# Kernel optimization log

Hardware: AMD Instinct MI355X
Metric: run time of the kernel (lower is better)

Reference implementation:

```python
import jax, jax.numpy as jnp
import numpy as np

N_NODES = 100000


def setup_inputs() -> dict:
    key = jax.random.key(0)
    k1, k2, k3, k4 = jax.random.split(key, 4)
    h = jax.random.normal(k1, (N_NODES, 128), dtype=jnp.float32)
    src = jax.random.randint(k2, (1600000,), 0, N_NODES, dtype=jnp.int32)
    dst = jax.random.randint(k3, (1600000,), 0, N_NODES, dtype=jnp.int32)
    # Linear params (PyTorch default init scale ~ 1/sqrt(in_feats))
    W = jax.random.normal(k4, (128, 128), dtype=jnp.float32) * (1.0 / np.sqrt(128.0))
    b = jnp.zeros((128,), dtype=jnp.float32)
    return {"h": h, "src": src, "dst": dst, "W": W, "b": b}


def reference(h, src, dst, W, b):
    # fn.copy_src: gather source-node features per edge  [E, F]
    msgs = h[src]
    # fn.sum: scatter-add messages into destination nodes  [N, F]
    agg = jax.ops.segment_sum(msgs, dst, num_segments=h.shape[0])
    # NodeUpdateModule: linear + relu
    out = agg @ W.T + b
    return jax.nn.relu(out)
```

## Files before the change

kernel.cpp:

```cpp
#include <hip/hip_runtime.h>

#define F      128
#define NPB    256
#define NPBS   8
#define NBMAX  512
#define ECAP   5120
#define CHMAX  4096
#define CH_PT  4
#define OVFCAP 32768
#define BR     64
#define KC     32

typedef short bf16x8 __attribute__((ext_vector_type(8)));
typedef float f32x4  __attribute__((ext_vector_type(4)));

__device__ __forceinline__ unsigned short f32_to_bf16_rne(float x) {
    unsigned u = __float_as_uint(x);
    u += 0x7fffu + ((u >> 16) & 1u);
    return (unsigned short)(u >> 16);
}

__global__ __launch_bounds__(256) void conv_w_kernel(
        const float* __restrict__ Wf, unsigned short* __restrict__ Wb, int n4) {
    int i = blockIdx.x * blockDim.x + threadIdx.x;
    if (i < n4) {
        float4 v = *(const float4*)(Wf + 4 * (long)i);
        ushort4 o;
        o.x = f32_to_bf16_rne(v.x);
        o.y = f32_to_bf16_rne(v.y);
        o.z = f32_to_bf16_rne(v.z);
        o.w = f32_to_bf16_rne(v.w);
        *(ushort4*)(Wb + 4 * (long)i) = o;
    }
}

__global__ __launch_bounds__(256) void gemm_h_kernel(
        const float* __restrict__ h,
        const unsigned short* __restrict__ Wb,
        unsigned short* __restrict__ hp,
        int n_rows) {
    __shared__ unsigned short a_lds[64][136];
    const int tid = threadIdx.x;
    const int r0 = blockIdx.x * 64;
    if (r0 >= n_rows) return;

    #pragma unroll
    for (int k = 0; k < 8; ++k) {
        int idx = k * 256 + tid;
        int row = idx >> 5;
        int c4 = idx & 31;
        int grow = min(r0 + row, n_rows - 1);
        float4 v = *(const float4*)(h + (long)grow * F + c4 * 4);
        ushort4 o;
        o.x = f32_to_bf16_rne(v.x);
        o.y = f32_to_bf16_rne(v.y);
        o.z = f32_to_bf16_rne(v.z);
        o.w = f32_to_bf16_rne(v.w);
        *(ushort4*)&a_lds[row][c4 * 4] = o;
    }
    __syncthreads();

    const int wv = tid >> 6;
    const int lane = tid & 63;
    const int mn = lane & 15;
    const int quad = lane >> 4;
    const int m0 = r0 + wv * 16;
    if (m0 >= n_rows) return;

    bf16x8 afr[4];
    #pragma unroll
    for (int kk = 0; kk < 4; ++kk)
        afr[kk] = *(const bf16x8*)&a_lds[wv * 16 + mn][kk * 32 + quad * 8];

    f32x4 acc[8];
    #pragma unroll
    for (int t = 0; t < 8; ++t) acc[t] = (f32x4){0.f, 0.f, 0.f, 0.f};

    #pragma unroll
    for (int kk = 0; kk < 4; ++kk) {
        #pragma unroll
        for (int t = 0; t < 8; ++t) {
            const unsigned short* wp = Wb + (long)(t * 16 + mn) * F + kk * 32 + quad * 8;
            bf16x8 bfr = *(const bf16x8*)wp;
            acc[t] = __builtin_amdgcn_mfma_f32_16x16x32_bf16(afr[kk], bfr, acc[t], 0, 0, 0);
        }
    }

    #pragma unroll
    for (int t = 0; t < 8; ++t) {
        const int col = t * 16 + mn;
        #pragma unroll
        for (int r = 0; r < 4; ++r) {
            const int orow = m0 + quad * 4 + r;
            if (orow < n_rows)
                hp[(long)orow * F + col] = f32_to_bf16_rne(acc[t][r]);
        }
    }
}

__global__ __launch_bounds__(1024) void count_kernel(
        const int* __restrict__ dst,
        int* __restrict__ cntmat,
        int n_edges, int NB) {
    __shared__ int hist[NBMAX];
    const int tid = threadIdx.x;
    const int lo = blockIdx.x * CHMAX;
    const int hi = min(n_edges, lo + CHMAX);
    for (int i = tid; i < NB; i += 1024) hist[i] = 0;
    __syncthreads();
    for (int i = lo + tid; i < hi; i += 1024)
        atomicAdd(&hist[((unsigned)dst[i]) >> NPBS], 1);
    __syncthreads();
    int* row = cntmat + (long)blockIdx.x * NB;
    for (int i = tid; i < NB; i += 1024) row[i] = hist[i];
}

__global__ __launch_bounds__(256) void scan_kernel(
        int* __restrict__ cntmat, int* __restrict__ gcnt, int NB, int NBLK) {
    __shared__ int wsum[4];
    const int b = blockIdx.x;
    const int tid = threadIdx.x;
    const int lane = tid & 63;
    const int w = tid >> 6;
    int carry = 0;
    for (int c0 = 0; c0 < NBLK; c0 += 256) {
        const int blk = c0 + tid;
        const int own = (blk < NBLK) ? cntmat[(long)blk * NB + b] : 0;
        int v = own;
        #pragma unroll
        for (int d = 1; d < 64; d <<= 1) { int u = __shfl_up(v, d); if (lane >= d) v += u; }
        if (lane == 63) wsum[w] = v;
        __syncthreads();
        if (w == 0) {
            int s = (lane < 4) ? wsum[lane] : 0;
            #pragma unroll
            for (int d = 1; d < 4; d <<= 1) { int u = __shfl_up(s, d); if (lane >= d) s += u; }
            if (lane < 4) wsum[lane] = s;
        }
        __syncthreads();
        const int excl = v - own + ((w > 0) ? wsum[w - 1] : 0) + carry;
        if (blk < NBLK) cntmat[(long)blk * NB + b] = excl;
        carry += wsum[3];
        __syncthreads();
    }
    if (tid == 0) gcnt[b] = carry;
}

__global__ __launch_bounds__(1024) void scatter_kernel(
        const int* __restrict__ src,
        const int* __restrict__ dst,
        const int* __restrict__ cntmat,
        int* __restrict__ ebuf,
        int* __restrict__ ovf,
        int n_edges, int NB) {
    __shared__ int hist[NBMAX];
    __shared__ int dlt[NBMAX];
    __shared__ int cursor[NBMAX];
    __shared__ int sval[CHMAX];
    __shared__ unsigned short sbkt[CHMAX];
    __shared__ int wsum[16];
    const int tid = threadIdx.x;
    const int lane = tid & 63;
    const int w = tid >> 6;
    const int lo = blockIdx.x * CHMAX;
    const int hi = min(n_edges, lo + CHMAX);
    const int len = hi - lo;

    int dd[CH_PT], ss[CH_PT];
    #pragma unroll
    for (int k = 0; k < CH_PT; ++k) {
        int i = lo + k * 1024 + tid;
        bool ok = i < hi;
        dd[k] = ok ? dst[i] : -1;
        ss[k] = ok ? src[i] : 0;
    }
    for (int i = tid; i < NB; i += 1024) hist[i] = 0;
    __syncthreads();

    #pragma unroll
    for (int k = 0; k < CH_PT; ++k)
        if (dd[k] >= 0) atomicAdd(&hist[((unsigned)dd[k]) >> NPBS], 1);
    __syncthreads();

    const int own = (tid < NB) ? hist[tid] : 0;
    int v = own;
    #pragma unroll
    for (int d = 1; d < 64; d <<= 1) { int u = __shfl_up(v, d); if (lane >= d) v += u; }
    if (lane == 63) wsum[w] = v;
    __syncthreads();
    if (w == 0) {
        int s = (lane < 16) ? wsum[lane] : 0;
        #pragma unroll
        for (int d = 1; d < 16; d <<= 1) { int u = __shfl_up(s, d); if (lane >= d) s += u; }
        if (lane < 16) wsum[lane] = s;
    }
    __syncthreads();
    if (tid < NB) {
        const int excl = v - own + ((w > 0) ? wsum[w - 1] : 0);
        dlt[tid] = cntmat[(long)blockIdx.x * NB + tid] - excl;
        cursor[tid] = excl;
    }
    __syncthreads();

    #pragma unroll
    for (int k = 0; k < CH_PT; ++k)
        if (dd[k] >= 0) {
            int b = ((unsigned)dd[k]) >> NPBS;
            int p = atomicAdd(&cursor[b], 1);
            sval[p] = ((dd[k] & (NPB - 1)) << 20) | ss[k];
            sbkt[p] = (unsigned short)b;
        }
    __syncthreads();

    for (int i = tid; i < len; i += 1024) {
        int vv = sval[i];
        int b = sbkt[i];
        int slot = i + dlt[b];
        if (slot < ECAP) {
            ebuf[(long)b * ECAP + slot] = vv;
        } else {
            int q = atomicAdd(&ovf[0], 1);
            if (q < OVFCAP) {
                ovf[1 + 2 * q] = (b << NPBS) | (vv >> 20);
                ovf[2 + 2 * q] = vv & 0xFFFFF;
            }
        }
    }
}

__global__ __launch_bounds__(1024) void bucket_gather_kernel(
        const unsigned short* __restrict__ hp,
        const int* __restrict__ gcnt,
        const int* __restrict__ ebuf,
        const int* __restrict__ ovf,
        const float* __restrict__ bias,
        float* __restrict__ out,
        int n_nodes) {
    __shared__ int hist[NPB];
    __shared__ int ofs[NPB];
    __shared__ int cur[NPB];
    __shared__ int srt[ECAP];
    __shared__ int wsum[16];
    const int bkt = blockIdx.x;
    const int tid = threadIdx.x;
    const int lane = tid & 63;
    const int w = tid >> 6;
    const int cnt = min(gcnt[bkt], ECAP);
    const int novf = ovf[0];
    const int* eb = ebuf + (long)bkt * ECAP;

    int ev[5];
    #pragma unroll
    for (int k = 0; k < 5; ++k) {
        int i = k * 1024 + tid;
        ev[k] = (i < cnt) ? eb[i] : -1;
    }
    if (tid < NPB) hist[tid] = 0;
    __syncthreads();

    #pragma unroll
    for (int k = 0; k < 5; ++k)
        if (ev[k] >= 0) atomicAdd(&hist[((unsigned)ev[k]) >> 20], 1);
    __syncthreads();

    const int own = (tid < NPB) ? hist[tid] : 0;
    int v = own;
    #pragma unroll
    for (int d = 1; d < 64; d <<= 1) { int u = __shfl_up(v, d); if (lane >= d) v += u; }
    if (lane == 63) wsum[w] = v;
    __syncthreads();
    if (w == 0) {
        int s = (lane < 16) ? wsum[lane] : 0;
        #pragma unroll
        for (int d = 1; d < 16; d <<= 1) { int u = __shfl_up(s, d); if (lane >= d) s += u; }
        if (lane < 16) wsum[lane] = s;
    }
    __syncthreads();
    if (tid < NPB) {
        const int e = v - own + ((w > 0) ? wsum[w - 1] : 0);
        ofs[tid] = e;
        cur[tid] = e;
    }
    __syncthreads();

    #pragma unroll
    for (int k = 0; k < 5; ++k)
        if (ev[k] >= 0) {
            int p = atomicAdd(&cur[((unsigned)ev[k]) >> 20], 1);
            srt[p] = ev[k] & 0xFFFFF;
        }
    __syncthreads();

    const unsigned lo4 = lane << 2;
    const float2 bv = *(const float2*)(bias + (lane << 1));
    for (int nl = w; nl < NPB; nl += 32) {
        const int nA = (bkt << NPBS) + nl;
        const int nB = nA + 16;
        if (nA >= n_nodes) break;
        const int begA = ofs[nl];
        const int lenA = hist[nl];
        const int begB = ofs[nl + 16];
        const int lenB = hist[nl + 16];
        const int fbA = (lenA > 0) ? begA : begB;
        const int fbB = (lenB > 0) ? begB : begA;
        const int mx = max(lenA, lenB);

        float ax0 = 0.f, ay0 = 0.f, ax1 = 0.f, ay1 = 0.f;
        for (int i = 0; i < mx; i += 8) {
            unsigned va[8], vb[8];
            bool la[8], lb[8];
            #pragma unroll
            for (int j = 0; j < 8; ++j) {
                la[j] = (i + j) < lenA;
                lb[j] = (i + j) < lenB;
                int sa = srt[la[j] ? begA + i + j : fbA];
                int sb = srt[lb[j] ? begB + i + j : fbB];
                va[j] = *(const unsigned*)((const char*)hp +
                                           (((unsigned)sa << 8) | lo4));
                vb[j] = *(const unsigned*)((const char*)hp +
                                           (((unsigned)sb << 8) | lo4));
            }
            #pragma unroll
            for (int j = 0; j < 8; ++j) {
                if (la[j]) {
                    ax0 += __uint_as_float(va[j] << 16);
                    ay0 += __uint_as_float(va[j] & 0xffff0000u);
                }
                if (lb[j]) {
                    ax1 += __uint_as_float(vb[j] << 16);
                    ay1 += __uint_as_float(vb[j] & 0xffff0000u);
                }
            }
        }

        if (novf > 0) {
            int ne = min(novf, OVFCAP);
            for (int k = 0; k < ne; ++k) {
                int dd = ovf[1 + 2 * k];
                if (dd == nA || dd == nB) {
                    unsigned u = *(const unsigned*)((const char*)hp +
                                   (((unsigned)ovf[2 + 2 * k] << 8) | lo4));
                    float ux = __uint_as_float(u << 16);
                    float uy = __uint_as_float(u & 0xffff0000u);
                    if (dd == nA) { ax0 += ux; ay0 += uy; }
                    else          { ax1 += ux; ay1 += uy; }
                }
            }
        }

        float rx0 = fmaxf(ax0 + bv.x, 0.f);
        float ry0 = fmaxf(ay0 + bv.y, 0.f);
        *(float2*)((char*)out + (((unsigned)nA << 9) | (lane << 3))) =
            make_float2(rx0, ry0);
        if (nB < n_nodes) {
            float rx1 = fmaxf(ax1 + bv.x, 0.f);
            float ry1 = fmaxf(ay1 + bv.y, 0.f);
            *(float2*)((char*)out + (((unsigned)nB << 9) | (lane << 3))) =
                make_float2(rx1, ry1);
        }
    }
}

__global__ void scatter_add_kernel(const float* __restrict__ h,
                                   const int* __restrict__ src,
                                   const int* __restrict__ dst,
                                   float* __restrict__ agg,
                                   long total) {
    long stride = (long)gridDim.x * blockDim.x;
    for (long i = (long)blockIdx.x * blockDim.x + threadIdx.x; i < total; i += stride) {
        int e    = (int)(i >> 5);
        int lane = (int)(i & 31);
        int s = src[e];
        int d = dst[e];
        float4 v = *(const float4*)(h + (long)s * F + (lane << 2));
        float* o = agg + (long)d * F + (lane << 2);
        unsafeAtomicAdd(o + 0, v.x);
        unsafeAtomicAdd(o + 1, v.y);
        unsafeAtomicAdd(o + 2, v.z);
        unsafeAtomicAdd(o + 3, v.w);
    }
}

__global__ __launch_bounds__(256) void gemm_bias_relu_inplace(
        float* __restrict__ out,
        const float* __restrict__ W,
        const float* __restrict__ bias,
        int n_rows) {
    __shared__ __align__(16) float a_t[KC][BR + 4];
    __shared__ __align__(16) float w_t[KC][F + 4];
    const int tid = threadIdx.x;
    const int tx = tid & 15;
    const int ty = tid >> 4;
    const int row0 = blockIdx.x * BR;
    float acc[4][8];
    #pragma unroll
    for (int i = 0; i < 4; ++i)
        #pragma unroll
        for (int j = 0; j < 8; ++j) acc[i][j] = 0.f;
    for (int kc = 0; kc < F; kc += KC) {
        #pragma unroll
        for (int p = 0; p < 2; ++p) {
            int q = tid + p * 256, r = q >> 3, kq = q & 7;
            int row = row0 + r;
            float4 v = make_float4(0.f, 0.f, 0.f, 0.f);
            if (row < n_rows) v = *(const float4*)(out + (long)row * F + kc + (kq << 2));
            a_t[kq * 4 + 0][r] = v.x; a_t[kq * 4 + 1][r] = v.y;
            a_t[kq * 4 + 2][r] = v.z; a_t[kq * 4 + 3][r] = v.w;
        }
        #pragma unroll
        for (int p = 0; p < 4; ++p) {
            int q = tid + p * 256, j = q >> 3, kq = q & 7;
            float4 v = *(const float4*)(W + (long)j * F + kc + (kq << 2));
            w_t[kq * 4 + 0][j] = v.x; w_t[kq * 4 + 1][j] = v.y;
            w_t[kq * 4 + 2][j] = v.z; w_t[kq * 4 + 3][j] = v.w;
        }
        __syncthreads();
        #pragma unroll
        for (int k = 0; k < KC; ++k) {
            float4 av = *(const float4*)&a_t[k][ty << 2];
            float4 w0 = *(const float4*)&w_t[k][tx << 2];
            float4 w1 = *(const float4*)&w_t[k][64 + (tx << 2)];
            float a4[4] = {av.x, av.y, av.z, av.w};
            float wv[8] = {w0.x, w0.y, w0.z, w0.w, w1.x, w1.y, w1.z, w1.w};
            #pragma unroll
            for (int i = 0; i < 4; ++i)
                #pragma unroll
                for (int j = 0; j < 8; ++j) acc[i][j] += a4[i] * wv[j];
        }
        __syncthreads();
    }
    float4 b0 = *(const float4*)(bias + (tx << 2));
    float4 b1 = *(const float4*)(bias + 64 + (tx << 2));
    #pragma unroll
    for (int i = 0; i < 4; ++i) {
        int row = row0 + (ty << 2) + i;
        if (row < n_rows) {
            float4 r0, r1;
            r0.x = fmaxf(acc[i][0] + b0.x, 0.f); r0.y = fmaxf(acc[i][1] + b0.y, 0.f);
            r0.z = fmaxf(acc[i][2] + b0.z, 0.f); r0.w = fmaxf(acc[i][3] + b0.w, 0.f);
            r1.x = fmaxf(acc[i][4] + b1.x, 0.f); r1.y = fmaxf(acc[i][5] + b1.y, 0.f);
            r1.z = fmaxf(acc[i][6] + b1.z, 0.f); r1.w = fmaxf(acc[i][7] + b1.w, 0.f);
            *(float4*)(out + (long)row * F + (tx << 2)) = r0;
            *(float4*)(out + (long)row * F + 64 + (tx << 2)) = r1;
        }
    }
}

extern "C" void kernel_launch(void* const* d_in, const int* in_sizes, int n_in,
                              void* d_out, int out_size, void* d_ws, size_t ws_size,
                              hipStream_t stream) {
    const float* h   = (const float*)d_in[0];
    const int*   src = (const int*)d_in[1];
    const int*   dst = (const int*)d_in[2];
    const float* W   = (const float*)d_in[3];
    const float* b   = (const float*)d_in[4];
    float* out = (float*)d_out;

    const int n_nodes = in_sizes[0] / F;
    const int n_edges = in_sizes[1];
    const int NB   = (n_nodes + NPB - 1) >> NPBS;
    const int NBLK = (n_edges + CHMAX - 1) / CHMAX;

    auto al16 = [](size_t x) { return (x + 15) & ~(size_t)15; };
    const size_t off_gcnt = 0;
    const size_t off_ovf  = al16((size_t)NB * 4);
    const size_t off_cmat = al16(off_ovf + 4 + (size_t)OVFCAP * 8);
    const size_t off_ebuf = al16(off_cmat + (size_t)NBLK * NB * 4);
    const size_t off_hp   = al16(off_ebuf + (size_t)NB * ECAP * 4);
    const size_t off_wb   = al16(off_hp + (size_t)n_nodes * F * 2);
    const size_t need     = off_wb + (size_t)F * F * 2;

    if (ws_size >= need && n_nodes > 0 && NB <= NBMAX) {
        int* gcnt = (int*)((char*)d_ws + off_gcnt);
        int* ovf  = (int*)((char*)d_ws + off_ovf);
        int* cmat = (int*)((char*)d_ws + off_cmat);
        int* ebuf = (int*)((char*)d_ws + off_ebuf);
        unsigned short* hp = (unsigned short*)((char*)d_ws + off_hp);
        unsigned short* Wb = (unsigned short*)((char*)d_ws + off_wb);

        hipMemsetAsync(ovf, 0, 4, stream);

        conv_w_kernel<<<(F * F / 4 + 255) / 256, 256, 0, stream>>>(W, Wb, F * F / 4);

        gemm_h_kernel<<<(n_nodes + 63) / 64, 256, 0, stream>>>(h, Wb, hp, n_nodes);

        if (NBLK > 0)
            count_kernel<<<NBLK, 1024, 0, stream>>>(dst, cmat, n_edges, NB);

        scan_kernel<<<NB, 256, 0, stream>>>(cmat, gcnt, NB, NBLK);

        if (NBLK > 0)
            scatter_kernel<<<NBLK, 1024, 0, stream>>>(src, dst, cmat, ebuf, ovf,
                                                      n_edges, NB);

        bucket_gather_kernel<<<NB, 1024, 0, stream>>>(hp, gcnt, ebuf, ovf, b,
                                                      out, n_nodes);
    } else {
        hipMemsetAsync(out, 0, (size_t)out_size * sizeof(float), stream);
        scatter_add_kernel<<<16384, 256, 0, stream>>>(
            h, src, dst, out, (long)n_edges * 32);
        const int gblocks = (n_nodes + BR - 1) / BR;
        gemm_bias_relu_inplace<<<gblocks, 256, 0, stream>>>(out, W, b, n_nodes);
    }
}
```

Baseline: 224.3 us.

## Fuse weight conversion and memset into count kernel; widen gather to 16-byte loads

```diff
diff --git a/kernel.cpp b/kernel.cpp
--- a/kernel.cpp
+++ b/kernel.cpp
@@ -20,18 +20,43 @@
     return (unsigned short)(u >> 16);
 }
 
-__global__ __launch_bounds__(256) void conv_w_kernel(
-        const float* __restrict__ Wf, unsigned short* __restrict__ Wb, int n4) {
-    int i = blockIdx.x * blockDim.x + threadIdx.x;
-    if (i < n4) {
-        float4 v = *(const float4*)(Wf + 4 * (long)i);
-        ushort4 o;
-        o.x = f32_to_bf16_rne(v.x);
-        o.y = f32_to_bf16_rne(v.y);
-        o.z = f32_to_bf16_rne(v.z);
-        o.w = f32_to_bf16_rne(v.w);
-        *(ushort4*)(Wb + 4 * (long)i) = o;
-    }
+__global__ __launch_bounds__(1024) void count_kernel(
+        const float* __restrict__ Wf,
+        unsigned short* __restrict__ Wb,
+        unsigned short* __restrict__ hp,
+        int* __restrict__ ovf,
+        const int* __restrict__ dst,
+        int* __restrict__ cntmat,
+        int n_edges, int NB, int n_nodes) {
+    const int tid = threadIdx.x;
+
+    if (blockIdx.x == 0) {
+        #pragma unroll
+        for (int k = 0; k < 4; ++k) {
+            int i = k * 1024 + tid;
+            float4 v = *(const float4*)(Wf + 4 * (long)i);
+            ushort4 o;
+            o.x = f32_to_bf16_rne(v.x);
+            o.y = f32_to_bf16_rne(v.y);
+            o.z = f32_to_bf16_rne(v.z);
+            o.w = f32_to_bf16_rne(v.w);
+            *(ushort4*)(Wb + 4 * (long)i) = o;
+        }
+        if (tid < 64) ((int*)(hp + (size_t)n_nodes * F))[tid] = 0;
+        if (tid == 0) ovf[0] = 0;
+        return;
+    }
+
+    __shared__ int hist[NBMAX];
+    const int lo = (blockIdx.x - 1) * CHMAX;
+    const int hi = min(n_edges, lo + CHMAX);
+    for (int i = tid; i < NB; i += 1024) hist[i] = 0;
+    __syncthreads();
+    for (int i = lo + tid; i < hi; i += 1024)
+        atomicAdd(&hist[((unsigned)dst[i]) >> NPBS], 1);
+    __syncthreads();
+    int* row = cntmat + (long)(blockIdx.x - 1) * NB;
+    for (int i = tid; i < NB; i += 1024) row[i] = hist[i];
 }
 
 __global__ __launch_bounds__(256) void gemm_h_kernel(
@@ -96,23 +121,6 @@
                 hp[(long)orow * F + col] = f32_to_bf16_rne(acc[t][r]);
         }
     }
-}
-
-__global__ __launch_bounds__(1024) void count_kernel(
-        const int* __restrict__ dst,
-        int* __restrict__ cntmat,
-        int n_edges, int NB) {
-    __shared__ int hist[NBMAX];
-    const int tid = threadIdx.x;
-    const int lo = blockIdx.x * CHMAX;
-    const int hi = min(n_edges, lo + CHMAX);
-    for (int i = tid; i < NB; i += 1024) hist[i] = 0;
-    __syncthreads();
-    for (int i = lo + tid; i < hi; i += 1024)
-        atomicAdd(&hist[((unsigned)dst[i]) >> NPBS], 1);
-    __syncthreads();
-    int* row = cntmat + (long)blockIdx.x * NB;
-    for (int i = tid; i < NB; i += 1024) row[i] = hist[i];
 }
 
 __global__ __launch_bounds__(256) void scan_kernel(
@@ -291,72 +299,80 @@
         }
     __syncthreads();
 
-    const unsigned lo4 = lane << 2;
-    const float2 bv = *(const float2*)(bias + (lane << 1));
-    for (int nl = w; nl < NPB; nl += 32) {
-        const int nA = (bkt << NPBS) + nl;
-        const int nB = nA + 16;
-        if (nA >= n_nodes) break;
-        const int begA = ofs[nl];
-        const int lenA = hist[nl];
-        const int begB = ofs[nl + 16];
-        const int lenB = hist[nl + 16];
-        const int fbA = (lenA > 0) ? begA : begB;
-        const int fbB = (lenB > 0) ? begB : begA;
-        const int mx = max(lenA, lenB);
-
-        float ax0 = 0.f, ay0 = 0.f, ax1 = 0.f, ay1 = 0.f;
-        for (int i = 0; i < mx; i += 8) {
-            unsigned va[8], vb[8];
-            bool la[8], lb[8];
+    const int li = lane & 15;
+    const int g  = lane >> 4;
+    const unsigned lob = (unsigned)li << 4;
+    const float4 bv0 = *(const float4*)(bias + li * 8);
+    const float4 bv1 = *(const float4*)(bias + li * 8 + 4);
+
+    for (int t = 0; t < 4; ++t) {
+        const int nl = w + 16 * (4 * t + g);
+        const int n = (bkt << NPBS) + nl;
+        const int beg = ofs[nl];
+        const int len = hist[nl];
+        int m1 = max(len, __shfl_xor(len, 16));
+        const int mx = max(m1, __shfl_xor(m1, 32));
+
+        float ax[8];
+        #pragma unroll
+        for (int q = 0; q < 8; ++q) ax[q] = 0.f;
+
+        for (int i = 0; i < mx; i += 4) {
+            uint4 vv[4];
             #pragma unroll
-            for (int j = 0; j < 8; ++j) {
-                la[j] = (i + j) < lenA;
-                lb[j] = (i + j) < lenB;
-                int sa = srt[la[j] ? begA + i + j : fbA];
-                int sb = srt[lb[j] ? begB + i + j : fbB];
-                va[j] = *(const unsigned*)((const char*)hp +
-                                           (((unsigned)sa << 8) | lo4));
-                vb[j] = *(const unsigned*)((const char*)hp +
-                                           (((unsigned)sb << 8) | lo4));
+            for (int j = 0; j < 4; ++j) {
+                const int e = i + j;
+                const bool val = e < len;
+                const int idx = val ? (beg + e) : 0;
+                int sr = srt[idx];
+                int sid = val ? sr : n_nodes;
+                vv[j] = *(const uint4*)((const char*)hp +
+                                        (((unsigned)sid << 8) | lob));
             }
             #pragma unroll
-            for (int j = 0; j < 8; ++j) {
-                if (la[j]) {
-                    ax0 += __uint_as_float(va[j] << 16);
-                    ay0 += __uint_as_float(va[j] & 0xffff0000u);
-                }
-                if (lb[j]) {
-                    ax1 += __uint_as_float(vb[j] << 16);
-                    ay1 += __uint_as_float(vb[j] & 0xffff0000u);
-                }
+            for (int j = 0; j < 4; ++j) {
+                ax[0] += __uint_as_float(vv[j].x << 16);
+                ax[1] += __uint_as_float(vv[j].x & 0xffff0000u);
+                ax[2] += __uint_as_float(vv[j].y << 16);
+                ax[3] += __uint_as_float(vv[j].y & 0xffff0000u);
+                ax[4] += __uint_as_float(vv[j].z << 16);
+                ax[5] += __uint_as_float(vv[j].z & 0xffff0000u);
+                ax[6] += __uint_as_float(vv[j].w << 16);
+                ax[7] += __uint_as_float(vv[j].w & 0xffff0000u);
             }
         }
 
         if (novf > 0) {
             int ne = min(novf, OVFCAP);
             for (int k = 0; k < ne; ++k) {
-                int dd = ovf[1 + 2 * k];
-                if (dd == nA || dd == nB) {
-                    unsigned u = *(const unsigned*)((const char*)hp +
-                                   (((unsigned)ovf[2 + 2 * k] << 8) | lo4));
-                    float ux = __uint_as_float(u << 16);
-                    float uy = __uint_as_float(u & 0xffff0000u);
-                    if (dd == nA) { ax0 += ux; ay0 += uy; }
-                    else          { ax1 += ux; ay1 += uy; }
+                if (ovf[1 + 2 * k] == n) {
+                    uint4 u = *(const uint4*)((const char*)hp +
+                               (((unsigned)ovf[2 + 2 * k] << 8) | lob));
+                    ax[0] += __uint_as_float(u.x << 16);
+                    ax[1] += __uint_as_float(u.x & 0xffff0000u);
+                    ax[2] += __uint_as_float(u.y << 16);
+                    ax[3] += __uint_as_float(u.y & 0xffff0000u);
+                    ax[4] += __uint_as_float(u.z << 16);
+                    ax[5] += __uint_as_float(u.z & 0xffff0000u);
+                    ax[6] += __uint_as_float(u.w << 16);
+                    ax[7] += __uint_as_float(u.w & 0xffff0000u);
                 }
             }
         }
 
-        float rx0 = fmaxf(ax0 + bv.x, 0.f);
-        float ry0 = fmaxf(ay0 + bv.y, 0.f);
-        *(float2*)((char*)out + (((unsigned)nA << 9) | (lane << 3))) =
-            make_float2(rx0, ry0);
-        if (nB < n_nodes) {
-            float rx1 = fmaxf(ax1 + bv.x, 0.f);
-            float ry1 = fmaxf(ay1 + bv.y, 0.f);
-            *(float2*)((char*)out + (((unsigned)nB << 9) | (lane << 3))) =
-                make_float2(rx1, ry1);
+        if (n < n_nodes) {
+            float4 r0, r1;
+            r0.x = fmaxf(ax[0] + bv0.x, 0.f);
+            r0.y = fmaxf(ax[1] + bv0.y, 0.f);
+            r0.z = fmaxf(ax[2] + bv0.z, 0.f);
+            r0.w = fmaxf(ax[3] + bv0.w, 0.f);
+            r1.x = fmaxf(ax[4] + bv1.x, 0.f);
+            r1.y = fmaxf(ax[5] + bv1.y, 0.f);
+            r1.z = fmaxf(ax[6] + bv1.z, 0.f);
+            r1.w = fmaxf(ax[7] + bv1.w, 0.f);
+            char* ob = (char*)out + (((unsigned)n << 9) | (lob << 1));
+            *(float4*)ob = r0;
+            *(float4*)(ob + 16) = r1;
         }
     }
 }
@@ -465,9 +481,9 @@
     const size_t off_gcnt = 0;
     const size_t off_ovf  = al16((size_t)NB * 4);
     const size_t off_cmat = al16(off_ovf + 4 + (size_t)OVFCAP * 8);
-    const size_t off_ebuf = al16(off_cmat + (size_t)NBLK * NB * 4);
+    const size_t off_ebuf = al16(off_cmat + (size_t)(NBLK > 0 ? NBLK : 1) * NB * 4);
     const size_t off_hp   = al16(off_ebuf + (size_t)NB * ECAP * 4);
-    const size_t off_wb   = al16(off_hp + (size_t)n_nodes * F * 2);
+    const size_t off_wb   = al16(off_hp + (size_t)(n_nodes + 1) * F * 2);
     const size_t need     = off_wb + (size_t)F * F * 2;
 
     if (ws_size >= need && n_nodes > 0 && NB <= NBMAX) {
@@ -478,14 +494,10 @@
         unsigned short* hp = (unsigned short*)((char*)d_ws + off_hp);
         unsigned short* Wb = (unsigned short*)((char*)d_ws + off_wb);
 
-        hipMemsetAsync(ovf, 0, 4, stream);
-
-        conv_w_kernel<<<(F * F / 4 + 255) / 256, 256, 0, stream>>>(W, Wb, F * F / 4);
+        count_kernel<<<NBLK + 1, 1024, 0, stream>>>(
+            W, Wb, hp, ovf, dst, cmat, n_edges, NB, n_nodes);
 
         gemm_h_kernel<<<(n_nodes + 63) / 64, 256, 0, stream>>>(h, Wb, hp, n_nodes);
-
-        if (NBLK > 0)
-            count_kernel<<<NBLK, 1024, 0, stream>>>(dst, cmat, n_edges, NB);
 
         scan_kernel<<<NB, 256, 0, stream>>>(cmat, gcnt, NB, NBLK);
 
```

After: 212.2 us. 1.06x faster.
